# Optimization experiments

Measured on AMD Instinct MI355X. Metric: run time of the kernel, lower is better.

Reference implementation:

```python
import jax, jax.numpy as jnp
import numpy as np

SELECTED_CLASS = 1  # matches init_kwargs


def _edt_sq(mask):
    """Exact squared Euclidean distance of each pixel to the nearest False pixel.
    Matches scipy.ndimage.distance_transform_edt(mask)**2 (2-pass separable,
    column scan + exact row-wise parabola minimization done brute-force in chunks).
    mask: (H, W) bool.
    """
    H, W = mask.shape
    BIG = np.float32(H + W)  # > any possible true distance, safe sentinel
    g = np.where(mask, BIG, np.float32(0.0)).astype(np.float32)
    for i in range(1, H):
        np.minimum(g[i], g[i - 1] + 1, out=g[i])
    for i in range(H - 2, -1, -1):
        np.minimum(g[i], g[i + 1] + 1, out=g[i])
    g2 = g * g  # (H, W) squared column distances
    k = np.arange(W, dtype=np.float32)
    d2 = np.empty((H, W), np.float32)
    CH = 64  # chunk of output columns to bound temp memory
    for j0 in range(0, W, CH):
        j = k[j0:j0 + CH]
        diff2 = (j[None, :] - k[:, None]) ** 2  # (W, Jc)
        d2[:, j0:j0 + CH] = (g2[:, :, None] + diff2[None]).min(axis=1)
    return d2


def _inner_boundary(mask):
    """skimage.segmentation.find_boundaries(mask, mode='inner'), connectivity=1:
    foreground pixels with at least one in-image 4-neighbor in background."""
    p = np.pad(mask, 1, constant_values=True)
    ero = p[1:-1, :-2] & p[1:-1, 2:] & p[:-2, 1:-1] & p[2:, 1:-1] & mask
    return mask & ~ero


def compute_sdf_np(y_true_sel):
    """Normalized signed distance map, faithful to BoundaryLoss.compute_sdf.
    y_true_sel: (B, 1, H, W) float; returns (B, 1, H, W) float32 in [-1, 1]."""
    masks = y_true_sel[:, 0].astype(bool)
    B, H, W = masks.shape
    out = np.zeros((B, 1, H, W), np.float32)
    for b in range(B):
        m = masks[b]
        if not m.any():
            continue  # original leaves zeros
        posdis = np.sqrt(_edt_sq(m))
        negdis = np.sqrt(_edt_sq(~m))
        sdf = (negdis - negdis.min()) / (negdis.max() - negdis.min()) \
            - (posdis - posdis.min()) / (posdis.max() - posdis.min())
        sdf[_inner_boundary(m)] = 0.0
        out[b, 0] = sdf
    return out


def setup_inputs():
    key = jax.random.key(0)
    k1, k2 = jax.random.split(key)
    B, C, H, W = 8, 4, 512, 512
    y_pred = jax.random.normal(k1, (B, C, H, W), dtype=jnp.float32)
    y_true = jax.random.randint(k2, (B, C, H, W), 0, 2).astype(jnp.float32)
    return {"y_pred": y_pred, "y_true": y_true}


def reference(y_pred, y_true):
    sel = SELECTED_CLASS
    # GT signed distance map (host-side, non-differentiable, as in the original
    # which round-trips through scipy on CPU): shape (B, 1, H, W)
    gt_sdf = jnp.asarray(compute_sdf_np(np.asarray(y_true[:, sel:sel + 1])))
    pc = jax.nn.sigmoid(y_pred)  # (B, C, H, W)
    # torch.einsum('bchw,bchw->bchw', pc, dc) with dc having c=1 broadcasts over C
    mult = pc * gt_sdf
    return mult.mean(axis=(1, 2, 3)).mean()
```

## Files before the change

### kernel.cpp

```cpp
#include <hip/hip_runtime.h>
#include <math.h>

#define B 8
#define C 4
#define H 512
#define W 512
#define SEL 1
#define BIGI 1024
#define NPIX (B*H*W)
#define CH 64
#define RC 8
#define TC 32
#define NSEG 16
#define LL 4
#define CINF 3000
#define G 4
#define NRU (B*H/G)

__global__ __launch_bounds__(512) void col_two_level(const float* __restrict__ ytrue,
                                                     unsigned short* __restrict__ gpk,
                                                     unsigned* __restrict__ sumsD,
                                                     unsigned* __restrict__ sumsU) {
    __shared__ int sP[NSEG][TC + 1], sN[NSEG][TC + 1];
    __shared__ int sCP[NSEG][TC + 1], sCN[NSEG][TC + 1];

    int blk = blockIdx.x;
    int b   = blk >> 7;
    int rem = blk & 127;
    int jt  = rem >> 3;
    int rc  = rem & 7;
    int tid = threadIdx.x;
    int tx  = tid & (TC - 1);
    int ty  = tid >> 5;
    int j   = jt * TC + tx;
    int i0  = rc * CH + ty * LL;

    const float* m = ytrue + ((size_t)b * C + SEL) * H * W + j;
    int gfp[LL], gfn[LL];
    int pp = BIGI, pn = BIGI;
    #pragma unroll
    for (int r = 0; r < LL; ++r) {
        bool fg = (m[(size_t)(i0 + r) * W] != 0.0f);
        int vp = fg ? BIGI : 0;
        int vn = fg ? 0 : BIGI;
        vp = min(vp, pp + 1); gfp[r] = vp; pp = vp;
        vn = min(vn, pn + 1); gfn[r] = vn; pn = vn;
    }
    sP[ty][tx] = pp - ty * LL;
    sN[ty][tx] = pn - ty * LL;
    __syncthreads();

    int col = tid >> 4, seg = tid & 15;
    int wp = sP[seg][col], wn = sN[seg][col];
    #pragma unroll
    for (int d = 1; d < NSEG; d <<= 1) {
        int a1 = __shfl_up(wp, d, 16);
        int a2 = __shfl_up(wn, d, 16);
        if (seg >= d) { wp = min(wp, a1); wn = min(wn, a2); }
    }
    if (seg < NSEG - 1) {
        sCP[seg + 1][col] = seg * LL + wp;
        sCN[seg + 1][col] = seg * LL + wn;
    } else {
        int jj = jt * TC + col;
        sumsD[((size_t)(b * RC + rc)) * W + jj] =
            (unsigned)(seg * LL + wp) | ((unsigned)(seg * LL + wn) << 16);
    }
    if (seg == 0) { sCP[0][col] = BIGI; sCN[0][col] = BIGI; }
    __syncthreads();

    int cp = sCP[ty][tx], cn = sCN[ty][tx];
    int lbp = 1 << 20, lbn = 1 << 20;
    #pragma unroll
    for (int r = 0; r < LL; ++r) {
        int vp = min(gfp[r], cp + 1 + r); gfp[r] = vp; lbp = min(lbp, vp + r);
        int vn = min(gfn[r], cn + 1 + r); gfn[r] = vn; lbn = min(lbn, vn + r);
    }
    sP[ty][tx] = lbp + ty * LL;
    sN[ty][tx] = lbn + ty * LL;
    __syncthreads();

    int w2p = sP[seg][col], w2n = sN[seg][col];
    #pragma unroll
    for (int d = 1; d < NSEG; d <<= 1) {
        int a1 = __shfl_down(w2p, d, 16);
        int a2 = __shfl_down(w2n, d, 16);
        if (seg + d < NSEG) { w2p = min(w2p, a1); w2n = min(w2n, a2); }
    }
    if (seg > 0) {
        sCP[seg - 1][col] = w2p - seg * LL;
        sCN[seg - 1][col] = w2n - seg * LL;
    } else {
        int jj = jt * TC + col;
        sumsU[((size_t)(b * RC + rc)) * W + jj] =
            (unsigned)w2p | ((unsigned)w2n << 16);
    }
    if (seg == NSEG - 1) { sCP[NSEG - 1][col] = BIGI; sCN[NSEG - 1][col] = BIGI; }
    __syncthreads();

    int pbp = sCP[ty][tx], pbn = sCN[ty][tx];
    unsigned short* op = gpk + ((size_t)b * H + i0) * W + j;
    #pragma unroll
    for (int r = LL - 1; r >= 0; --r) {
        int vp = min(gfp[r], pbp + 1); pbp = vp;
        int vn = min(gfn[r], pbn + 1); pbn = vn;
        int fg = (vn == 0) ? 1 : 0;
        int g2 = vp + vn;
        op[(size_t)r * W] = (unsigned short)((g2 << 1) | fg);
    }
}

__global__ __launch_bounds__(512) void row_fused(const unsigned short* __restrict__ gpk,
                                                 const unsigned* __restrict__ sumsD,
                                                 const unsigned* __restrict__ sumsU,
                                                 const float* __restrict__ ypred,
                                                 float* __restrict__ rowpart) {
    __shared__ float s1[G][W];
    __shared__ float sw[4][8];

    int blk = blockIdx.x;
    int b = blk >> 7;
    int g = blk & 127;
    int i0 = g * G;
    int rc = i0 >> 6;
    int j = threadIdx.x;

    int Ap = CINF, An = CINF, Bp = CINF, Bn = CINF;
    #pragma unroll
    for (int q = 0; q < RC; ++q) {
        if (q < rc) {
            unsigned dv = sumsD[((size_t)(b * RC + q)) * W + j];
            int e = q * CH + CH - 1;
            Ap = min(Ap, (int)(dv & 0xFFFFu) - e);
            An = min(An, (int)(dv >> 16) - e);
        } else if (q > rc) {
            unsigned uv = sumsU[((size_t)(b * RC + q)) * W + j];
            int s0 = q * CH;
            Bp = min(Bp, (int)(uv & 0xFFFFu) + s0);
            Bn = min(Bn, (int)(uv >> 16) + s0);
        }
    }

    #pragma unroll
    for (int r = 0; r < G; ++r) {
        int ii = i0 + r;
        unsigned v = gpk[((size_t)b * H + ii) * W + j];
        int fg = v & 1;
        int gv = v >> 1;
        int gp = fg ? gv : 0;
        int gn = fg ? 0 : gv;
        gp = min(gp, min(Ap + ii, Bp - ii));
        gn = min(gn, min(An + ii, Bn - ii));
        int gg = gp + gn;
        float sv = (float)(gg * gg);
        s1[r][j] = fg ? sv : -sv;
    }
    __syncthreads();

    float mxp = 0.f, mxn = 0.f, A = 0.f, Bv = 0.f;
    #pragma unroll
    for (int r = 0; r < G; ++r) {
        float sv = s1[r][j];
        bool fg = (sv > 0.f);
        float sgn = fg ? 1.f : -1.f;
        float bq = fabsf(sv);
        for (int rr = 1; rr < W; ++rr) {
            float r2 = (float)(rr * rr);
            if (r2 >= bq) break;
            int jl = j - rr, jr = j + rr;
            if (jl >= 0) { float u = s1[r][jl]; bq = fminf(bq, fmaxf(u * sgn, 0.f) + r2); }
            if (jr < W)  { float u = s1[r][jr]; bq = fminf(bq, fmaxf(u * sgn, 0.f) + r2); }
        }
        float d = sqrtf(bq);
        bool bnd = fg && (bq == 1.0f);

        const float* yp = ypred + ((size_t)b * C * H + i0 + r) * W + j;
        float s = 0.f;
        #pragma unroll
        for (int cc = 0; cc < C; ++cc) {
            float x = yp[(size_t)cc * H * W];
            s += 1.0f / (1.0f + __expf(-x));
        }
        float se = bnd ? 0.f : s;
        mxp = fmaxf(mxp, fg ? bq : 0.f);
        mxn = fmaxf(mxn, fg ? 0.f : bq);
        A  += fg ? se * d : 0.f;
        Bv += fg ? 0.f : se * d;
    }

    for (int off = 32; off >= 1; off >>= 1) {
        mxp = fmaxf(mxp, __shfl_down(mxp, off));
        mxn = fmaxf(mxn, __shfl_down(mxn, off));
        A  += __shfl_down(A, off);
        Bv += __shfl_down(Bv, off);
    }
    int wave = threadIdx.x >> 6, lane = threadIdx.x & 63;
    if (lane == 0) { sw[0][wave] = mxp; sw[1][wave] = mxn; sw[2][wave] = A; sw[3][wave] = Bv; }
    __syncthreads();
    if (threadIdx.x == 0) {
        float a0 = sw[0][0], a1 = sw[1][0], a2 = sw[2][0], a3 = sw[3][0];
        #pragma unroll
        for (int w = 1; w < 8; ++w) {
            a0 = fmaxf(a0, sw[0][w]); a1 = fmaxf(a1, sw[1][w]);
            a2 += sw[2][w]; a3 += sw[3][w];
        }
        *(float4*)(rowpart + (size_t)blk * 4) = make_float4(a0, a1, a2, a3);
    }
}

__global__ __launch_bounds__(512) void batch_final(const float* __restrict__ rowpart,
                                                   float* __restrict__ out) {
    __shared__ double sacc[8];
    int bw = threadIdx.x >> 6;
    int lane = threadIdx.x & 63;
    const float4* rv = (const float4*)(rowpart + (size_t)bw * 128 * 4);
    float4 e0 = rv[lane];
    float4 e1 = rv[lane + 64];
    float mxp = fmaxf(e0.x, e1.x), mxn = fmaxf(e0.y, e1.y);
    float A = e0.z + e1.z, Bv = e0.w + e1.w;
    for (int off = 32; off >= 1; off >>= 1) {
        mxp = fmaxf(mxp, __shfl_down(mxp, off));
        mxn = fmaxf(mxn, __shfl_down(mxn, off));
        A  += __shfl_down(A, off);
        Bv += __shfl_down(Bv, off);
    }
    if (lane == 0) {
        float pmax = sqrtf(mxp), nmax = sqrtf(mxn);
        float invp = (pmax > 0.f) ? 1.0f / pmax : 0.0f;
        float invn = (nmax > 0.f) ? 1.0f / nmax : 0.0f;
        sacc[bw] = (pmax > 0.f) ? (double)(invn * Bv - invp * A) : 0.0;
    }
    __syncthreads();
    if (threadIdx.x == 0) {
        double tt = 0.0;
        #pragma unroll
        for (int q = 0; q < 8; ++q) tt += sacc[q];
        out[0] = (float)(tt / (double)((size_t)B * C * H * W));
    }
}

extern "C" void kernel_launch(void* const* d_in, const int* in_sizes, int n_in,
                              void* d_out, int out_size, void* d_ws, size_t ws_size,
                              hipStream_t stream) {
    const float* ypred = (const float*)d_in[0];
    const float* ytrue = (const float*)d_in[1];
    float* out = (float*)d_out;

    unsigned short* gpk = (unsigned short*)d_ws;
    unsigned* sumsD = (unsigned*)(gpk + NPIX);
    unsigned* sumsU = sumsD + (size_t)B * RC * W;
    float* rowpart = (float*)(sumsU + (size_t)B * RC * W);

    col_two_level<<<B * 16 * RC, 512, 0, stream>>>(ytrue, gpk, sumsD, sumsU);
    row_fused<<<NRU, 512, 0, stream>>>(gpk, sumsD, sumsU, ypred, rowpart);
    batch_final<<<1, 512, 0, stream>>>(rowpart, out);
}
```

Baseline: 25.16 us.

## Pack four rows per column into ushort4 and peel first parabola steps

The intermediate column-distance buffer is stored interleaved so each thread writes and reads its four consecutive rows as a single ushort4, replacing four strided 16-bit accesses. The row kernel keeps its own values in registers and unrolls the first two neighbour offsets with clamped indices, so the search loop starts at distance three and updates the squared radius incrementally. The goal is fewer memory transactions and less loop overhead. The write pattern in the column kernel changes from row-major coalesced shorts to 8-byte strided vectors.

```diff
diff --git a/kernel.cpp b/kernel.cpp
--- a/kernel.cpp
+++ b/kernel.cpp
@@ -18,7 +18,7 @@
 #define NRU (B*H/G)
 
 __global__ __launch_bounds__(512) void col_two_level(const float* __restrict__ ytrue,
-                                                     unsigned short* __restrict__ gpk,
+                                                     unsigned short* __restrict__ gpkT,
                                                      unsigned* __restrict__ sumsD,
                                                      unsigned* __restrict__ sumsU) {
     __shared__ int sP[NSEG][TC + 1], sN[NSEG][TC + 1];
@@ -99,18 +99,20 @@
     __syncthreads();
 
     int pbp = sCP[ty][tx], pbn = sCN[ty][tx];
-    unsigned short* op = gpk + ((size_t)b * H + i0) * W + j;
+    unsigned short g4[LL];
     #pragma unroll
     for (int r = LL - 1; r >= 0; --r) {
         int vp = min(gfp[r], pbp + 1); pbp = vp;
         int vn = min(gfn[r], pbn + 1); pbn = vn;
         int fg = (vn == 0) ? 1 : 0;
         int g2 = vp + vn;
-        op[(size_t)r * W] = (unsigned short)((g2 << 1) | fg);
-    }
-}
-
-__global__ __launch_bounds__(512) void row_fused(const unsigned short* __restrict__ gpk,
+        g4[r] = (unsigned short)((g2 << 1) | fg);
+    }
+    ushort4 pk; pk.x = g4[0]; pk.y = g4[1]; pk.z = g4[2]; pk.w = g4[3];
+    *(ushort4*)(gpkT + (((size_t)b * (H / 4) + (i0 >> 2)) * W + j) * 4) = pk;
+}
+
+__global__ __launch_bounds__(512) void row_fused(const unsigned short* __restrict__ gpkT,
                                                  const unsigned* __restrict__ sumsD,
                                                  const unsigned* __restrict__ sumsU,
                                                  const float* __restrict__ ypred,
@@ -125,26 +127,31 @@
     int rc = i0 >> 6;
     int j = threadIdx.x;
 
+    const unsigned* sd = sumsD + (size_t)b * RC * W + j;
+    const unsigned* su = sumsU + (size_t)b * RC * W + j;
     int Ap = CINF, An = CINF, Bp = CINF, Bn = CINF;
     #pragma unroll
     for (int q = 0; q < RC; ++q) {
         if (q < rc) {
-            unsigned dv = sumsD[((size_t)(b * RC + q)) * W + j];
+            unsigned dv = sd[(size_t)q * W];
             int e = q * CH + CH - 1;
             Ap = min(Ap, (int)(dv & 0xFFFFu) - e);
             An = min(An, (int)(dv >> 16) - e);
         } else if (q > rc) {
-            unsigned uv = sumsU[((size_t)(b * RC + q)) * W + j];
+            unsigned uv = su[(size_t)q * W];
             int s0 = q * CH;
             Bp = min(Bp, (int)(uv & 0xFFFFu) + s0);
             Bn = min(Bn, (int)(uv >> 16) + s0);
         }
     }
 
+    const ushort4 v4 = *(const ushort4*)(gpkT + (((size_t)b * (H / 4) + g) * W + j) * 4);
+    unsigned short vv[4] = { v4.x, v4.y, v4.z, v4.w };
+    float svr[G];
     #pragma unroll
     for (int r = 0; r < G; ++r) {
         int ii = i0 + r;
-        unsigned v = gpk[((size_t)b * H + ii) * W + j];
+        unsigned v = vv[r];
         int fg = v & 1;
         int gv = v >> 1;
         int gp = fg ? gv : 0;
@@ -153,23 +160,34 @@
         gn = min(gn, min(An + ii, Bn - ii));
         int gg = gp + gn;
         float sv = (float)(gg * gg);
-        s1[r][j] = fg ? sv : -sv;
-    }
-    __syncthreads();
+        sv = fg ? sv : -sv;
+        svr[r] = sv;
+        s1[r][j] = sv;
+    }
+    __syncthreads();
+
+    int jl1 = (j >= 1) ? j - 1 : j, jr1 = (j < W - 1) ? j + 1 : j;
+    int jl2 = (j >= 2) ? j - 2 : j, jr2 = (j < W - 2) ? j + 2 : j;
 
     float mxp = 0.f, mxn = 0.f, A = 0.f, Bv = 0.f;
     #pragma unroll
     for (int r = 0; r < G; ++r) {
-        float sv = s1[r][j];
+        float sv = svr[r];
         bool fg = (sv > 0.f);
         float sgn = fg ? 1.f : -1.f;
         float bq = fabsf(sv);
-        for (int rr = 1; rr < W; ++rr) {
-            float r2 = (float)(rr * rr);
+        float u1 = s1[r][jl1], u2 = s1[r][jr1], u3 = s1[r][jl2], u4 = s1[r][jr2];
+        bq = fminf(bq, fmaxf(u1 * sgn, 0.f) + 1.f);
+        bq = fminf(bq, fmaxf(u2 * sgn, 0.f) + 1.f);
+        bq = fminf(bq, fmaxf(u3 * sgn, 0.f) + 4.f);
+        bq = fminf(bq, fmaxf(u4 * sgn, 0.f) + 4.f);
+        float r2 = 9.f, drr = 7.f;
+        for (int rr = 3; rr < W; ++rr) {
             if (r2 >= bq) break;
             int jl = j - rr, jr = j + rr;
             if (jl >= 0) { float u = s1[r][jl]; bq = fminf(bq, fmaxf(u * sgn, 0.f) + r2); }
             if (jr < W)  { float u = s1[r][jr]; bq = fminf(bq, fmaxf(u * sgn, 0.f) + r2); }
+            r2 += drr; drr += 2.f;
         }
         float d = sqrtf(bq);
         bool bnd = fg && (bq == 1.0f);
@@ -246,12 +264,12 @@
     const float* ytrue = (const float*)d_in[1];
     float* out = (float*)d_out;
 
-    unsigned short* gpk = (unsigned short*)d_ws;
-    unsigned* sumsD = (unsigned*)(gpk + NPIX);
+    unsigned short* gpkT = (unsigned short*)d_ws;
+    unsigned* sumsD = (unsigned*)(gpkT + NPIX);
     unsigned* sumsU = sumsD + (size_t)B * RC * W;
     float* rowpart = (float*)(sumsU + (size_t)B * RC * W);
 
-    col_two_level<<<B * 16 * RC, 512, 0, stream>>>(ytrue, gpk, sumsD, sumsU);
-    row_fused<<<NRU, 512, 0, stream>>>(gpk, sumsD, sumsU, ypred, rowpart);
+    col_two_level<<<B * 16 * RC, 512, 0, stream>>>(ytrue, gpkT, sumsD, sumsU);
+    row_fused<<<NRU, 512, 0, stream>>>(gpkT, sumsD, sumsU, ypred, rowpart);
     batch_final<<<1, 512, 0, stream>>>(rowpart, out);
 }
```

Result: faster. 24.61 us (-2.2%).
